# Kernel tuning notes

Measured on AMD Instinct MI355X. Metric: run time of the kernel, lower is better.

## Reference

```python
import jax, jax.numpy as jnp
import numpy as np
from jax import lax

# dims: B=2, C=dim=64, H=W=128 -> N=16384 tokens; d_inner=128, d_state=16, dt_rank=4, d_conv=4

def setup_inputs() -> dict:
    key = jax.random.key(0)
    ks = jax.random.split(key, 8)
    def n(k, shp, scale=0.02):
        return jax.random.normal(k, shp, jnp.float32) * scale
    d_inner, d_state, dt_rank = 128, 16, 4
    return {
        "x": jax.random.normal(ks[0], (2, 64, 128, 128), jnp.float32),
        "ln_w": jnp.ones((64,), jnp.float32),
        "ln_b": jnp.zeros((64,), jnp.float32),
        "in_proj_w": n(ks[1], (2 * d_inner, 64)),
        "conv_w": n(ks[2], (d_inner, 1, 4), 0.1),
        "conv_b": jnp.zeros((d_inner,), jnp.float32),
        "x_proj_w": n(ks[3], (dt_rank + 2 * d_state, d_inner)),
        "dt_proj_w": n(ks[4], (d_inner, dt_rank), 0.5),
        "dt_proj_b": n(ks[5], (d_inner,), 0.1),
        "A_log": jnp.log(jnp.broadcast_to(jnp.arange(1, d_state + 1, dtype=jnp.float32), (d_inner, d_state))),
        "D_param": jnp.ones((d_inner,), jnp.float32),
        "out_proj_w": n(ks[6], (64, d_inner)),
        "out_proj_b": jnp.zeros((64,), jnp.float32),
    }


def reference(x, ln_w, ln_b, in_proj_w, conv_w, conv_b, x_proj_w,
              dt_proj_w, dt_proj_b, A_log, D_param, out_proj_w, out_proj_b):
    B, C, H, W = x.shape
    d_inner = in_proj_w.shape[0] // 2
    d_state = A_log.shape[1]
    dt_rank = dt_proj_w.shape[1]
    eps = 1e-5

    # feature2token + channel LayerNorm (Restormer WithBias LN over C)
    t = x.reshape(B, C, H * W).transpose(0, 2, 1)  # [B, N, C]
    mu = jnp.mean(t, axis=-1, keepdims=True)
    var = jnp.var(t, axis=-1, keepdims=True)
    t = (t - mu) * lax.rsqrt(var + eps) * ln_w + ln_b

    # in_proj -> x, z
    xz = jnp.einsum('bnc,dc->bnd', t, in_proj_w)  # [B, N, 2*d_inner]
    x_in, z = jnp.split(xz, 2, axis=-1)

    # depthwise causal conv1d (k=4, pad left 3), then SiLU
    u = lax.conv_general_dilated(
        x_in.transpose(0, 2, 1), conv_w,
        window_strides=(1,), padding=[(3, 0)],
        feature_group_count=d_inner,
        dimension_numbers=('NCH', 'OIH', 'NCH'))
    u = jax.nn.silu(u + conv_b[None, :, None]).transpose(0, 2, 1)  # [B, N, d_inner]

    # x_proj -> dt, B, C of the SSM
    x_dbl = jnp.einsum('bnd,ed->bne', u, x_proj_w)
    dt_r = x_dbl[..., :dt_rank]
    Bmat = x_dbl[..., dt_rank:dt_rank + d_state]   # [B, N, d_state]
    Cmat = x_dbl[..., dt_rank + d_state:]          # [B, N, d_state]
    dt = jax.nn.softplus(jnp.einsum('bnr,dr->bnd', dt_r, dt_proj_w) + dt_proj_b)

    # selective scan: h_t = exp(dt*A) h_{t-1} + dt*B*u
    A = -jnp.exp(A_log)  # [d_inner, d_state]
    deltaA = jnp.exp(jnp.einsum('bnd,ds->bnds', dt, A))
    deltaBu = jnp.einsum('bnd,bns,bnd->bnds', dt, Bmat, u)

    def combine(c1, c2):
        a1, b1 = c1
        a2, b2 = c2
        return a2 * a1, a2 * b1 + b2

    _, h = lax.associative_scan(combine, (deltaA, deltaBu), axis=1)  # h: [B, N, d_inner, d_state]

    y = jnp.einsum('bnds,bns->bnd', h, Cmat) + u * D_param
    y = y * jax.nn.silu(z)
    out = jnp.einsum('bnd,cd->bnc', y, out_proj_w) + out_proj_b  # [B, N, C]

    # token2feature
    return out.transpose(0, 2, 1).reshape(B, C, H, W)
```

## Files before the change

### kernel.cpp

```cpp
#include <hip/hip_runtime.h>
#include <math.h>

#define NTOK 16384
#define DIN  128
#define NCH  512
#define CHL  32
#define NG   16

__device__ __forceinline__ float silu_f(float x)    { return x / (1.f + __expf(-x)); }
__device__ __forceinline__ float softplus_f(float x){ return (x > 20.f) ? x : log1pf(__expf(x)); }

__global__ __launch_bounds__(256) void k1_ln_inproj(
    const float* __restrict__ x, const float* __restrict__ lnw,
    const float* __restrict__ lnb, const float* __restrict__ Win,
    float* __restrict__ xin, float* __restrict__ zbuf)
{
  __shared__ __align__(16) float tl[64*68];
  __shared__ __align__(16) float wt[64*132];
  __shared__ float ps[256], pq[256], mu[64], rs[64];

  int t = threadIdx.x;
  int lane = t & 63, grp = t >> 6;
  int b  = blockIdx.x >> 8;
  int n0 = (blockIdx.x & 255) << 6;
  const float* xb = x + ((size_t)b * 64) * NTOK;

  for (int i = 0; i < 16; ++i) {
    int c = grp*16 + i;
    tl[c*68 + lane] = xb[(size_t)c*NTOK + n0 + lane];
  }
  __syncthreads();
  float s0 = 0.f, s1 = 0.f;
  for (int i = 0; i < 16; ++i) {
    float v = tl[(grp*16+i)*68 + lane];
    s0 += v; s1 += v*v;
  }
  ps[t] = s0; pq[t] = s1;
  __syncthreads();
  if (t < 64) {
    float m = ps[t] + ps[64+t] + ps[128+t] + ps[192+t];
    float q = pq[t] + pq[64+t] + pq[128+t] + pq[192+t];
    m *= 0.015625f;
    q = q*0.015625f - m*m;
    mu[t] = m; rs[t] = rsqrtf(q + 1e-5f);
  }
  __syncthreads();
  for (int i = 0; i < 16; ++i) {
    int idx = (i<<8) + t;
    int c = idx >> 6, j = idx & 63;
    tl[c*68 + j] = (tl[c*68 + j] - mu[j]) * rs[j] * lnw[c] + lnb[c];
  }

  int dl = t & 127, drow = t >> 7;
  int d0 = (lane & 31) << 2;
  int joff = grp*8 + ((lane >> 5) << 2);
  for (int half = 0; half < 2; ++half) {
    __syncthreads();
    for (int i = 0; i < 32; ++i) {
      int c = drow*32 + i;
      wt[c*132 + dl] = Win[((half<<7) + dl)*64 + c];
    }
    __syncthreads();
    for (int p = 0; p < 2; ++p) {
      int jb = joff + (p << 5);
      float acc[4][4] = {{0.f}};
      #pragma unroll 8
      for (int c = 0; c < 64; ++c) {
        float4 tv = *(const float4*)&tl[c*68 + jb];
        float4 wv = *(const float4*)&wt[c*132 + d0];
        acc[0][0] += tv.x*wv.x; acc[0][1] += tv.x*wv.y; acc[0][2] += tv.x*wv.z; acc[0][3] += tv.x*wv.w;
        acc[1][0] += tv.y*wv.x; acc[1][1] += tv.y*wv.y; acc[1][2] += tv.y*wv.z; acc[1][3] += tv.y*wv.w;
        acc[2][0] += tv.z*wv.x; acc[2][1] += tv.z*wv.y; acc[2][2] += tv.z*wv.z; acc[2][3] += tv.z*wv.w;
        acc[3][0] += tv.w*wv.x; acc[3][1] += tv.w*wv.y; acc[3][2] += tv.w*wv.z; acc[3][3] += tv.w*wv.w;
      }
      #pragma unroll
      for (int jj = 0; jj < 4; ++jj) {
        long n = (long)b*NTOK + n0 + jb + jj;
        float4 o = make_float4(acc[jj][0], acc[jj][1], acc[jj][2], acc[jj][3]);
        if (half == 0) {
          *(float4*)&xin[n*128 + d0] = o;
        } else {
          o.x = silu_f(o.x); o.y = silu_f(o.y); o.z = silu_f(o.z); o.w = silu_f(o.w);
          *(float4*)&zbuf[n*128 + d0] = o;
        }
      }
    }
  }
}

__global__ __launch_bounds__(256) void k2_conv(
    const float* __restrict__ xin, const float* __restrict__ cw,
    const float* __restrict__ cb, float* __restrict__ u)
{
  int t = threadIdx.x;
  int d = t & 127;
  long g = (long)blockIdx.x*2 + (t >> 7);
  int n  = (int)(g & (NTOK-1));
  float acc = cb[d];
  #pragma unroll
  for (int k = 0; k < 4; ++k) {
    int m = n - 3 + k;
    if (m >= 0) acc += cw[d*4 + k] * xin[(g - 3 + k)*128 + d];
  }
  u[g*128 + d] = silu_f(acc);
}

__global__ __launch_bounds__(256) void k3_xproj_dt(
    const float* __restrict__ u, const float* __restrict__ Wx,
    const float* __restrict__ Wdt, const float* __restrict__ db,
    float* __restrict__ dt, float* __restrict__ Bm, float* __restrict__ Cm)
{
  __shared__ __align__(16) float wx[36*128];
  __shared__ float wdtT[4*128];
  __shared__ __align__(16) float xdbl[64*40];
  int t = threadIdx.x;
  for (int i = t; i < 1152; i += 256)
    *(float4*)&wx[i*4] = *(const float4*)&Wx[i*4];
  for (int i = t; i < 512; i += 256)
    wdtT[(i&3)*128 + (i>>2)] = Wdt[i];
  __syncthreads();

  long tok0 = (long)blockIdx.x * 64;
  int tok = t & 63, grp = t >> 6;
  const float* urow = u + (tok0 + tok)*128;

  float acc[9];
  #pragma unroll
  for (int e = 0; e < 9; ++e) acc[e] = 0.f;
  #pragma unroll 8
  for (int d4 = 0; d4 < 32; ++d4) {
    float4 uv = *(const float4*)&urow[d4*4];
    #pragma unroll
    for (int e = 0; e < 9; ++e) {
      float4 wv = *(const float4*)&wx[(grp*9+e)*128 + d4*4];
      acc[e] += uv.x*wv.x + uv.y*wv.y + uv.z*wv.z + uv.w*wv.w;
    }
  }
  #pragma unroll
  for (int e = 0; e < 9; ++e) xdbl[tok*40 + grp*9 + e] = acc[e];
  __syncthreads();

  {
    int tk = t >> 2, q = t & 3;
    float4 bv = *(const float4*)&xdbl[tk*40 + 4  + q*4];
    float4 cv = *(const float4*)&xdbl[tk*40 + 20 + q*4];
    *(float4*)&Bm[(tok0+tk)*16 + q*4] = bv;
    *(float4*)&Cm[(tok0+tk)*16 + q*4] = cv;
  }
  int d = t & 127, th = t >> 7;
  float w0 = wdtT[d], w1 = wdtT[128+d], w2 = wdtT[256+d], w3 = wdtT[384+d];
  float bias = db[d];
  for (int j = 0; j < 32; ++j) {
    int tk = th*32 + j;
    float a = bias + xdbl[tk*40]*w0 + xdbl[tk*40+1]*w1
                   + xdbl[tk*40+2]*w2 + xdbl[tk*40+3]*w3;
    dt[(tok0+tk)*128 + d] = softplus_f(a);
  }
}

__global__ __launch_bounds__(128) void k4a_local(
    const float* __restrict__ dt, const float* __restrict__ u,
    const float* __restrict__ Bm, const float* __restrict__ Alog,
    float* __restrict__ carP, float* __restrict__ carH)
{
  int d = threadIdx.x;
  int b = blockIdx.x / NCH, ch = blockIdx.x % NCH;
  long nb = (long)b*NTOK + (long)ch*CHL;
  float A[16], h[16], P[16];
  #pragma unroll
  for (int k = 0; k < 4; ++k) {
    float4 a = *(const float4*)&Alog[d*16 + k*4];
    A[k*4+0] = -__expf(a.x); A[k*4+1] = -__expf(a.y);
    A[k*4+2] = -__expf(a.z); A[k*4+3] = -__expf(a.w);
  }
  #pragma unroll
  for (int s = 0; s < 16; ++s) { h[s] = 0.f; P[s] = 1.f; }
  for (int i = 0; i < CHL; ++i) {
    long n = nb + i;
    float dtv = dt[n*128 + d];
    float uv  = u [n*128 + d];
    float du  = dtv * uv;
    float Bv[16];
    #pragma unroll
    for (int k = 0; k < 4; ++k) {
      float4 v = *(const float4*)&Bm[n*16 + k*4];
      Bv[k*4]=v.x; Bv[k*4+1]=v.y; Bv[k*4+2]=v.z; Bv[k*4+3]=v.w;
    }
    #pragma unroll
    for (int s = 0; s < 16; ++s) {
      float dA = __expf(dtv * A[s]);
      h[s] = dA*h[s] + du*Bv[s];
      P[s] *= dA;
    }
  }
  long cbs = ((long)(b*NCH + ch)*128 + d) * 16;
  #pragma unroll
  for (int k = 0; k < 4; ++k) {
    *(float4*)&carP[cbs + k*4] = make_float4(P[k*4],P[k*4+1],P[k*4+2],P[k*4+3]);
    *(float4*)&carH[cbs + k*4] = make_float4(h[k*4],h[k*4+1],h[k*4+2],h[k*4+3]);
  }
}

__global__ __launch_bounds__(256) void k4b1_group(
    float* __restrict__ cP, float* __restrict__ cH,
    float* __restrict__ Pg, float* __restrict__ Hg)
{
  int idx = blockIdx.x*256 + threadIdx.x;
  int rem = idx & 2047;
  int g   = (idx >> 11) & (NG-1);
  int b   = idx >> 15;
  float P = 1.f, H = 0.f;
  long base = ((long)b*NCH + g*32)*2048 + rem;
  for (int j = 0; j < 32; ++j) {
    long a = base + (long)j*2048;
    float p = cP[a], h = cH[a];
    cP[a] = P; cH[a] = H;
    H = p*H + h;
    P = p*P;
  }
  long ga = ((long)b*NG + g)*2048 + rem;
  Pg[ga] = P; Hg[ga] = H;
}

__global__ __launch_bounds__(256) void k4b2_carry(
    const float* __restrict__ Pg, float* __restrict__ Hg)
{
  int idx = blockIdx.x*256 + threadIdx.x;
  int b = idx >> 11, rem = idx & 2047;
  float H = 0.f;
  for (int g = 0; g < NG; ++g) {
    long a = ((long)b*NG + g)*2048 + rem;
    float p = Pg[a], h = Hg[a];
    Hg[a] = H;
    H = p*H + h;
  }
}

__global__ __launch_bounds__(128) void k4c_apply(
    const float* __restrict__ dt, const float* __restrict__ u,
    const float* __restrict__ Bm, const float* __restrict__ Cm,
    const float* __restrict__ Alog, const float* __restrict__ Dp,
    const float* __restrict__ zs, const float* __restrict__ pPre,
    const float* __restrict__ hPre, const float* __restrict__ Hg,
    float* __restrict__ yz)
{
  int d = threadIdx.x;
  int b = blockIdx.x / NCH, ch = blockIdx.x % NCH;
  long nb = (long)b*NTOK + (long)ch*CHL;
  float A[16], h[16];
  #pragma unroll
  for (int k = 0; k < 4; ++k) {
    float4 a = *(const float4*)&Alog[d*16 + k*4];
    A[k*4+0] = -__expf(a.x); A[k*4+1] = -__expf(a.y);
    A[k*4+2] = -__expf(a.z); A[k*4+3] = -__expf(a.w);
  }
  long cbs = ((long)(b*NCH + ch)*128 + d) * 16;
  long gbs = ((long)b*NG + (ch >> 5))*2048 + d*16;
  #pragma unroll
  for (int k = 0; k < 4; ++k) {
    float4 hp = *(const float4*)&hPre[cbs + k*4];
    float4 pp = *(const float4*)&pPre[cbs + k*4];
    float4 gi = *(const float4*)&Hg[gbs + k*4];
    h[k*4+0] = hp.x + pp.x*gi.x; h[k*4+1] = hp.y + pp.y*gi.y;
    h[k*4+2] = hp.z + pp.z*gi.z; h[k*4+3] = hp.w + pp.w*gi.w;
  }
  float Dv = Dp[d];
  for (int i = 0; i < CHL; ++i) {
    long n = nb + i;
    float dtv = dt[n*128 + d];
    float uv  = u [n*128 + d];
    float du  = dtv * uv;
    float Bv[16], Cv[16];
    #pragma unroll
    for (int k = 0; k < 4; ++k) {
      float4 v = *(const float4*)&Bm[n*16 + k*4];
      Bv[k*4]=v.x; Bv[k*4+1]=v.y; Bv[k*4+2]=v.z; Bv[k*4+3]=v.w;
      float4 w = *(const float4*)&Cm[n*16 + k*4];
      Cv[k*4]=w.x; Cv[k*4+1]=w.y; Cv[k*4+2]=w.z; Cv[k*4+3]=w.w;
    }
    float y = 0.f;
    #pragma unroll
    for (int s = 0; s < 16; ++s) {
      float dA = __expf(dtv * A[s]);
      h[s] = dA*h[s] + du*Bv[s];
      y += h[s]*Cv[s];
    }
    y = (y + uv*Dv) * zs[n*128 + d];
    yz[n*128 + d] = y;
  }
}

__global__ __launch_bounds__(256) void k6_outproj(
    const float* __restrict__ yz, const float* __restrict__ Wout,
    const float* __restrict__ ob, float* __restrict__ out)
{
  __shared__ __align__(16) float wo[64*132];
  __shared__ __align__(16) float yl[32*132];
  int t = threadIdx.x;
  long tok0 = (long)blockIdx.x * 32;
  for (int i = 0; i < 8; ++i) {
    int g = i*256 + t; int c = g >> 5, q = g & 31;
    *(float4*)&wo[c*132 + q*4] = *(const float4*)&Wout[c*128 + q*4];
  }
  for (int i = 0; i < 4; ++i) {
    int g = i*256 + t; int tok = g >> 5, q = g & 31;
    *(float4*)&yl[tok*132 + q*4] = *(const float4*)&yz[(tok0 + tok)*128 + q*4];
  }
  __syncthreads();
  int tp = t & 15;
  int tg = t >> 4;
  float acc[4][2] = {{0.f}};
  for (int d4 = 0; d4 < 32; ++d4) {
    float4 y0 = *(const float4*)&yl[tg*132 + d4*4];
    float4 y1 = *(const float4*)&yl[(tg+16)*132 + d4*4];
    #pragma unroll
    for (int cc = 0; cc < 4; ++cc) {
      float4 wv = *(const float4*)&wo[(tp + 16*cc)*132 + d4*4];
      acc[cc][0] += wv.x*y0.x + wv.y*y0.y + wv.z*y0.z + wv.w*y0.w;
      acc[cc][1] += wv.x*y1.x + wv.y*y1.y + wv.z*y1.z + wv.w*y1.w;
    }
  }
  int b  = (int)(tok0 / NTOK);
  long n0 = tok0 % NTOK;
  #pragma unroll
  for (int cc = 0; cc < 4; ++cc) {
    int c = tp + 16*cc;
    float bias = ob[c];
    out[((long)b*64 + c)*NTOK + n0 + tg     ] = acc[cc][0] + bias;
    out[((long)b*64 + c)*NTOK + n0 + tg + 16] = acc[cc][1] + bias;
  }
}

extern "C" void kernel_launch(void* const* d_in, const int* in_sizes, int n_in,
                              void* d_out, int out_size, void* d_ws, size_t ws_size,
                              hipStream_t stream)
{
  (void)in_sizes; (void)n_in; (void)out_size; (void)ws_size;
  const float* x    = (const float*)d_in[0];
  const float* lnw  = (const float*)d_in[1];
  const float* lnb  = (const float*)d_in[2];
  const float* Win  = (const float*)d_in[3];
  const float* cw   = (const float*)d_in[4];
  const float* cb   = (const float*)d_in[5];
  const float* Wx   = (const float*)d_in[6];
  const float* Wdt  = (const float*)d_in[7];
  const float* db   = (const float*)d_in[8];
  const float* Alog = (const float*)d_in[9];
  const float* Dp   = (const float*)d_in[10];
  const float* Wout = (const float*)d_in[11];
  const float* ob   = (const float*)d_in[12];
  float* out = (float*)d_out;

  float* w   = (float*)d_ws;
  float* xin = w;
  float* z   = w + 4194304;
  float* u   = w + 8388608;
  float* dt  = w + 12582912;
  float* Bm  = w + 16777216;
  float* Cm  = w + 17301504;
  float* cP  = w + 17825792;
  float* cH  = w + 19922944;
  float* Pg  = w + 22020096;
  float* Hg  = w + 22085632;

  k1_ln_inproj<<<512,  256, 0, stream>>>(x, lnw, lnb, Win, xin, z);
  k2_conv     <<<16384,256, 0, stream>>>(xin, cw, cb, u);
  k3_xproj_dt <<<512,  256, 0, stream>>>(u, Wx, Wdt, db, dt, Bm, Cm);
  k4a_local   <<<1024, 128, 0, stream>>>(dt, u, Bm, Alog, cP, cH);
  k4b1_group  <<<256,  256, 0, stream>>>(cP, cH, Pg, Hg);
  k4b2_carry  <<<16,   256, 0, stream>>>(Pg, Hg);
  k4c_apply   <<<1024, 128, 0, stream>>>(dt, u, Bm, Cm, Alog, Dp, z, cP, cH, Hg, xin);
  k6_outproj  <<<1024, 256, 0, stream>>>(xin, Wout, ob, out);
}
```

Baseline: 164.4 us.

## Retile in-proj GEMM, batch conv per thread, split carry scan into more groups

The LN+in_proj kernel now fuses the x load with the statistics pass and transposes the normalized tile into token-major shared memory. The GEMM becomes a 4x8 register tile over float4 channel chunks, with weights stored d-major in a reused buffer. The conv kernel has each thread slide a 4-tap window over 8 consecutive tokens, which cuts redundant global reads and the block count. The chunk-carry scan uses 32 groups of 16 chunks instead of 16 of 32, giving more parallelism in the group pass but a longer serial carry pass. The new GEMM also writes scalar, strided outputs, which may coalesce less well than the previous float4 stores.

```diff
diff --git a/kernel.cpp b/kernel.cpp
--- a/kernel.cpp
+++ b/kernel.cpp
@@ -5,7 +5,8 @@
 #define DIN  128
 #define NCH  512
 #define CHL  32
-#define NG   16
+#define NG   32
+#define GCH  16
 
 __device__ __forceinline__ float silu_f(float x)    { return x / (1.f + __expf(-x)); }
 __device__ __forceinline__ float softplus_f(float x){ return (x > 20.f) ? x : log1pf(__expf(x)); }
@@ -15,24 +16,21 @@
     const float* __restrict__ lnb, const float* __restrict__ Win,
     float* __restrict__ xin, float* __restrict__ zbuf)
 {
-  __shared__ __align__(16) float tl[64*68];
-  __shared__ __align__(16) float wt[64*132];
+  __shared__ __align__(16) float bufA[128*68];
+  __shared__ __align__(16) float bufB[64*68];
   __shared__ float ps[256], pq[256], mu[64], rs[64];
 
   int t = threadIdx.x;
-  int lane = t & 63, grp = t >> 6;
   int b  = blockIdx.x >> 8;
   int n0 = (blockIdx.x & 255) << 6;
-  const float* xb = x + ((size_t)b * 64) * NTOK;
-
-  for (int i = 0; i < 16; ++i) {
-    int c = grp*16 + i;
-    tl[c*68 + lane] = xb[(size_t)c*NTOK + n0 + lane];
-  }
-  __syncthreads();
+  const float* xb = x + ((size_t)b*64)*NTOK;
+
+  int tok = t & 63, quad = t >> 6;
   float s0 = 0.f, s1 = 0.f;
   for (int i = 0; i < 16; ++i) {
-    float v = tl[(grp*16+i)*68 + lane];
+    int c = i*4 + quad;
+    float v = xb[(size_t)c*NTOK + n0 + tok];
+    bufA[c*68 + tok] = v;
     s0 += v; s1 += v*v;
   }
   ps[t] = s0; pq[t] = s1;
@@ -45,44 +43,62 @@
     mu[t] = m; rs[t] = rsqrtf(q + 1e-5f);
   }
   __syncthreads();
-  for (int i = 0; i < 16; ++i) {
-    int idx = (i<<8) + t;
-    int c = idx >> 6, j = idx & 63;
-    tl[c*68 + j] = (tl[c*68 + j] - mu[j]) * rs[j] * lnw[c] + lnb[c];
-  }
-
-  int dl = t & 127, drow = t >> 7;
-  int d0 = (lane & 31) << 2;
-  int joff = grp*8 + ((lane >> 5) << 2);
+
+  {
+    int c = t & 63, tq = t >> 6;
+    float wv = lnw[c], bv = lnb[c];
+    const float4* A4 = (const float4*)bufA;
+    #pragma unroll
+    for (int i = 0; i < 4; ++i) {
+      int tok4 = tq*4 + i;
+      float4 f = A4[c*17 + tok4];
+      float vals[4] = {f.x, f.y, f.z, f.w};
+      #pragma unroll
+      for (int k = 0; k < 4; ++k) {
+        int tk = tok4*4 + k;
+        bufB[tk*68 + c] = (vals[k] - mu[tk]) * rs[tk] * wv + bv;
+      }
+    }
+  }
+
+  int tokg = t & 15, dg = t >> 4;
   for (int half = 0; half < 2; ++half) {
     __syncthreads();
     for (int i = 0; i < 32; ++i) {
-      int c = drow*32 + i;
-      wt[c*132 + dl] = Win[((half<<7) + dl)*64 + c];
+      int idx = i*256 + t;
+      int c = idx & 63, dd = idx >> 6;
+      bufA[dd*68 + c] = Win[((half<<7) + dd)*64 + c];
     }
     __syncthreads();
-    for (int p = 0; p < 2; ++p) {
-      int jb = joff + (p << 5);
-      float acc[4][4] = {{0.f}};
-      #pragma unroll 8
-      for (int c = 0; c < 64; ++c) {
-        float4 tv = *(const float4*)&tl[c*68 + jb];
-        float4 wv = *(const float4*)&wt[c*132 + d0];
-        acc[0][0] += tv.x*wv.x; acc[0][1] += tv.x*wv.y; acc[0][2] += tv.x*wv.z; acc[0][3] += tv.x*wv.w;
-        acc[1][0] += tv.y*wv.x; acc[1][1] += tv.y*wv.y; acc[1][2] += tv.y*wv.z; acc[1][3] += tv.y*wv.w;
-        acc[2][0] += tv.z*wv.x; acc[2][1] += tv.z*wv.y; acc[2][2] += tv.z*wv.z; acc[2][3] += tv.z*wv.w;
-        acc[3][0] += tv.w*wv.x; acc[3][1] += tv.w*wv.y; acc[3][2] += tv.w*wv.z; acc[3][3] += tv.w*wv.w;
-      }
-      #pragma unroll
-      for (int jj = 0; jj < 4; ++jj) {
-        long n = (long)b*NTOK + n0 + jb + jj;
-        float4 o = make_float4(acc[jj][0], acc[jj][1], acc[jj][2], acc[jj][3]);
-        if (half == 0) {
-          *(float4*)&xin[n*128 + d0] = o;
-        } else {
-          o.x = silu_f(o.x); o.y = silu_f(o.y); o.z = silu_f(o.z); o.w = silu_f(o.w);
-          *(float4*)&zbuf[n*128 + d0] = o;
-        }
+    float acc[4][8];
+    #pragma unroll
+    for (int i = 0; i < 4; ++i)
+      #pragma unroll
+      for (int j = 0; j < 8; ++j) acc[i][j] = 0.f;
+    const float4* TB = (const float4*)bufB;
+    const float4* WA = (const float4*)bufA;
+    #pragma unroll 4
+    for (int c4 = 0; c4 < 16; ++c4) {
+      float4 tv[4], wv[8];
+      #pragma unroll
+      for (int i = 0; i < 4; ++i) tv[i] = TB[(tokg + 16*i)*17 + c4];
+      #pragma unroll
+      for (int j = 0; j < 8; ++j) wv[j] = WA[(dg + 16*j)*17 + c4];
+      #pragma unroll
+      for (int i = 0; i < 4; ++i)
+        #pragma unroll
+        for (int j = 0; j < 8; ++j)
+          acc[i][j] += tv[i].x*wv[j].x + tv[i].y*wv[j].y
+                     + tv[i].z*wv[j].z + tv[i].w*wv[j].w;
+    }
+    #pragma unroll
+    for (int i = 0; i < 4; ++i) {
+      long n = (long)b*NTOK + n0 + tokg + 16*i;
+      #pragma unroll
+      for (int j = 0; j < 8; ++j) {
+        int d = dg + 16*j;
+        if (half == 0) xin[n*128 + d] = acc[i][j];
+        else           zbuf[n*128 + d] = silu_f(acc[i][j]);
       }
     }
   }
@@ -94,15 +110,19 @@
 {
   int t = threadIdx.x;
   int d = t & 127;
-  long g = (long)blockIdx.x*2 + (t >> 7);
-  int n  = (int)(g & (NTOK-1));
-  float acc = cb[d];
-  #pragma unroll
-  for (int k = 0; k < 4; ++k) {
-    int m = n - 3 + k;
-    if (m >= 0) acc += cw[d*4 + k] * xin[(g - 3 + k)*128 + d];
-  }
-  u[g*128 + d] = silu_f(acc);
+  long g0 = (long)blockIdx.x*16 + (t >> 7)*8;
+  int n = (int)(g0 & (NTOK-1));
+  float w0 = cw[d*4], w1 = cw[d*4+1], w2 = cw[d*4+2], w3 = cw[d*4+3];
+  float cbv = cb[d];
+  float xa = (n >= 3) ? xin[(g0-3)*128 + d] : 0.f;
+  float xb = (n >= 2) ? xin[(g0-2)*128 + d] : 0.f;
+  float xc = (n >= 1) ? xin[(g0-1)*128 + d] : 0.f;
+  #pragma unroll
+  for (int j = 0; j < 8; ++j) {
+    float xd = xin[(g0+j)*128 + d];
+    u[(g0+j)*128 + d] = silu_f(w0*xa + w1*xb + w2*xc + w3*xd + cbv);
+    xa = xb; xb = xc; xc = xd;
+  }
 }
 
 __global__ __launch_bounds__(256) void k3_xproj_dt(
@@ -208,10 +228,11 @@
   int idx = blockIdx.x*256 + threadIdx.x;
   int rem = idx & 2047;
   int g   = (idx >> 11) & (NG-1);
-  int b   = idx >> 15;
+  int b   = idx >> 16;
   float P = 1.f, H = 0.f;
-  long base = ((long)b*NCH + g*32)*2048 + rem;
-  for (int j = 0; j < 32; ++j) {
+  long base = ((long)b*NCH + g*GCH)*2048 + rem;
+  #pragma unroll 4
+  for (int j = 0; j < GCH; ++j) {
     long a = base + (long)j*2048;
     float p = cP[a], h = cH[a];
     cP[a] = P; cH[a] = H;
@@ -228,6 +249,7 @@
   int idx = blockIdx.x*256 + threadIdx.x;
   int b = idx >> 11, rem = idx & 2047;
   float H = 0.f;
+  #pragma unroll 4
   for (int g = 0; g < NG; ++g) {
     long a = ((long)b*NG + g)*2048 + rem;
     float p = Pg[a], h = Hg[a];
@@ -255,7 +277,7 @@
     A[k*4+2] = -__expf(a.z); A[k*4+3] = -__expf(a.w);
   }
   long cbs = ((long)(b*NCH + ch)*128 + d) * 16;
-  long gbs = ((long)b*NG + (ch >> 5))*2048 + d*16;
+  long gbs = ((long)b*NG + (ch >> 4))*2048 + d*16;
   #pragma unroll
   for (int k = 0; k < 4; ++k) {
     float4 hp = *(const float4*)&hPre[cbs + k*4];
@@ -361,14 +383,14 @@
   float* cP  = w + 17825792;
   float* cH  = w + 19922944;
   float* Pg  = w + 22020096;
-  float* Hg  = w + 22085632;
-
-  k1_ln_inproj<<<512,  256, 0, stream>>>(x, lnw, lnb, Win, xin, z);
-  k2_conv     <<<16384,256, 0, stream>>>(xin, cw, cb, u);
-  k3_xproj_dt <<<512,  256, 0, stream>>>(u, Wx, Wdt, db, dt, Bm, Cm);
-  k4a_local   <<<1024, 128, 0, stream>>>(dt, u, Bm, Alog, cP, cH);
-  k4b1_group  <<<256,  256, 0, stream>>>(cP, cH, Pg, Hg);
-  k4b2_carry  <<<16,   256, 0, stream>>>(Pg, Hg);
-  k4c_apply   <<<1024, 128, 0, stream>>>(dt, u, Bm, Cm, Alog, Dp, z, cP, cH, Hg, xin);
-  k6_outproj  <<<1024, 256, 0, stream>>>(xin, Wout, ob, out);
-}
+  float* Hg  = w + 22151168;
+
+  k1_ln_inproj<<<512, 256, 0, stream>>>(x, lnw, lnb, Win, xin, z);
+  k2_conv     <<<2048,256, 0, stream>>>(xin, cw, cb, u);
+  k3_xproj_dt <<<512, 256, 0, stream>>>(u, Wx, Wdt, db, dt, Bm, Cm);
+  k4a_local   <<<1024,128, 0, stream>>>(dt, u, Bm, Alog, cP, cH);
+  k4b1_group  <<<512, 256, 0, stream>>>(cP, cH, Pg, Hg);
+  k4b2_carry  <<<16,  256, 0, stream>>>(Pg, Hg);
+  k4c_apply   <<<1024,128, 0, stream>>>(dt, u, Bm, Cm, Alog, Dp, z, cP, cH, Hg, xin);
+  k6_outproj  <<<1024,256, 0, stream>>>(xin, Wout, ob, out);
+}
```

After: 158.0 us. -3.9%, faster.
